# Optimization experiments

Hardware: AMD Instinct MI355X
Metric: run time of the kernel (lower is better)

## Reference

```python
import jax, jax.numpy as jnp
import numpy as np

N, E, F_IN, D, L = 100000, 1600000, 32, 128, 5
B, V, T, EMB = 3000, 64, 128, 64
H = L * D  # 640 LSTM hidden
BN_EPS = 1e-5


def setup_inputs():
    key = jax.random.key(0)
    ks = jax.random.split(key, 20)
    rn = lambda k, s, sc=0.05: jax.random.normal(k, s, jnp.float32) * sc
    inp = {
        'x': jax.random.normal(ks[0], (N, F_IN), jnp.float32),
        'edge_index': jax.random.randint(ks[1], (2, E), 0, N, jnp.int32),
        'batch': jnp.sort(jax.random.randint(ks[2], (N,), 0, B, jnp.int32)),
        'smi': jax.random.randint(ks[3], (B, T), 0, V, jnp.int32),
        'gin0_w1': rn(ks[4], (F_IN, D)), 'gin0_b1': jnp.zeros((D,), jnp.float32),
        'gin0_w2': rn(ks[5], (D, D)),    'gin0_b2': jnp.zeros((D,), jnp.float32),
        'ginr_w1': rn(ks[6], (L - 1, D, D)), 'ginr_b1': jnp.zeros((L - 1, D), jnp.float32),
        'ginr_w2': rn(ks[7], (L - 1, D, D)), 'ginr_b2': jnp.zeros((L - 1, D), jnp.float32),
        'bn_gamma': jnp.ones((L, D), jnp.float32), 'bn_beta': jnp.zeros((L, D), jnp.float32),
        'emb': rn(ks[8], (V, EMB), 0.1).at[0].set(0.0),  # padding_idx=0
        'w_ih': rn(ks[9], (4 * H, EMB), 0.04), 'w_hh': rn(ks[10], (4 * H, H), 0.04),
        'b_ih': jnp.zeros((4 * H,), jnp.float32), 'b_hh': jnp.zeros((4 * H,), jnp.float32),
        'g_w1': rn(ks[11], (L * D, 4 * D)), 'g_b1': jnp.zeros((4 * D,), jnp.float32),
        'g_bn_gamma': jnp.ones((4 * D,), jnp.float32), 'g_bn_beta': jnp.zeros((4 * D,), jnp.float32),
        'g_w2': rn(ks[12], (4 * D, 6 * D)),
    }
    return inp


def _bn(h, gamma, beta):
    # BatchNorm1d in training mode: biased batch statistics
    mu = h.mean(0)
    var = h.var(0)
    return (h - mu) * jax.lax.rsqrt(var + BN_EPS) * gamma + beta


def _gin_layer(h, src, dst, w1, b1, w2, b2, gamma, beta):
    # GINConv (eps=0): MLP(x + sum_{j->i} x_j), then ReLU, then BN
    agg = jax.ops.segment_sum(h[src], dst, num_segments=N)  # [N, d]
    z = h + agg
    z = jnp.maximum(z @ w1 + b1, 0.0) @ w2 + b2
    z = jnp.maximum(z, 0.0)
    return _bn(z, gamma, beta)


def _lstm_last(e, w_ih, w_hh, b_ih, b_hh):
    # e: [B, T, EMB] -> last hidden state [B, H]
    def step(carry, xt):
        h, c = carry
        gates = xt @ w_ih.T + b_ih + h @ w_hh.T + b_hh  # [B, 4H]
        i, f, g, o = jnp.split(gates, 4, axis=1)  # torch gate order i,f,g,o
        c = jax.nn.sigmoid(f) * c + jax.nn.sigmoid(i) * jnp.tanh(g)
        h = jax.nn.sigmoid(o) * jnp.tanh(c)
        return (h, c), None
    h0 = jnp.zeros((e.shape[0], H), e.dtype)
    (h, _), _ = jax.lax.scan(step, (h0, h0), e.transpose(1, 0, 2))
    return h


def reference(x, edge_index, batch, smi, gin0_w1, gin0_b1, gin0_w2, gin0_b2,
              ginr_w1, ginr_b1, ginr_w2, ginr_b2, bn_gamma, bn_beta, emb,
              w_ih, w_hh, b_ih, b_hh, g_w1, g_b1, g_bn_gamma, g_bn_beta, g_w2):
    src, dst = edge_index[0], edge_index[1]
    # --- GIN encoder with layer-wise global_add_pool ---
    h = _gin_layer(x, src, dst, gin0_w1, gin0_b1, gin0_w2, gin0_b2, bn_gamma[0], bn_beta[0])
    pools = [jax.ops.segment_sum(h, batch, num_segments=B)]
    for i in range(L - 1):
        h = _gin_layer(h, src, dst, ginr_w1[i], ginr_b1[i], ginr_w2[i], ginr_b2[i],
                       bn_gamma[i + 1], bn_beta[i + 1])
        pools.append(jax.ops.segment_sum(h, batch, num_segments=B))
    enc1 = jnp.concatenate(pools, axis=1)  # [B, L*D]
    # --- SMILES encoder: Embedding + LSTM, take output at last timestep ---
    enc2 = _lstm_last(emb[smi], w_ih, w_hh, b_ih, b_hh)  # [B, H] == [B, L*D]
    # --- shared projection head g, L2-normalized (F.normalize, eps=1e-12) ---
    def g_head(z):
        z1 = jnp.maximum(_bn(z @ g_w1 + g_b1, g_bn_gamma, g_bn_beta), 0.0)
        out = z1 @ g_w2
        nrm = jnp.maximum(jnp.linalg.norm(out, axis=1, keepdims=True), 1e-12)
        return out / nrm
    return (g_head(enc1), g_head(enc2))
```

## Files before the change

kernel.cpp:

```cpp
#include <hip/hip_runtime.h>

typedef __bf16 bf16x8 __attribute__((ext_vector_type(8)));
typedef float f32x4 __attribute__((ext_vector_type(4)));
typedef unsigned short ushort8 __attribute__((ext_vector_type(8)));

#define DEV static __device__ __forceinline__

DEV unsigned short f2bf(float f){
  unsigned int u = __builtin_bit_cast(unsigned int, f);
  u += 0x7fffu + ((u >> 16) & 1u);
  return (unsigned short)(u >> 16);
}
DEV float bf2f(unsigned short u){
  return __builtin_bit_cast(float, ((unsigned int)u) << 16);
}
DEV float sigf(float x){ return 1.0f/(1.0f + __expf(-x)); }
DEV float tanhf_fast(float x){
  float ax = fabsf(x);
  float e = __expf(2.0f*ax);
  float r = 1.0f - 2.0f/(e + 1.0f);
  return copysignf(r, x);
}

static constexpr int NN   = 100000;
static constexpr int NPAD = 100096;
static constexpr int NE   = 1600000;
static constexpr int NB   = 3000;
static constexpr int BPAD = 3072;
static constexpr int TT   = 128;
static constexpr int HID  = 640;
static constexpr int SCAN_B = 1024;
static constexpr int NBLK = (NN + SCAN_B - 1)/SCAN_B;

__global__ void cvt_k(const float* __restrict__ s, unsigned short* __restrict__ d, int n){
  int i = blockIdx.x*256 + threadIdx.x; if (i < n) d[i] = f2bf(s[i]);
}
__global__ void transpose_cvt_split_k(const float* __restrict__ s, unsigned short* __restrict__ dh,
                                      unsigned short* __restrict__ dl, int R, int C){
  int i = blockIdx.x*256 + threadIdx.x; if (i >= R*C) return;
  int r = i / C, c = i - r*C;
  float v = s[i];
  unsigned short hi = f2bf(v);
  dh[c*R + r] = hi;
  dl[c*R + r] = f2bf(v - bf2f(hi));
}
__global__ void wc2_build_k(const float* __restrict__ whh, const float* __restrict__ wih,
                            unsigned short* __restrict__ wc2){
  int i = blockIdx.x*256 + threadIdx.x; if (i >= 2560*704) return;
  int n2 = i / 704, k = i - n2*704;
  int jt = n2 >> 7, rem = n2 & 127;
  int hc = rem >> 6, gate = (rem >> 4) & 3, j15 = rem & 15;
  int n = gate*640 + jt*32 + hc*16 + j15;
  float v = (k < 640) ? whh[n*640 + k] : wih[n*64 + (k - 640)];
  wc2[i] = f2bf(v);
}
__global__ void add_k(const float* __restrict__ a, const float* __restrict__ b, float* __restrict__ o, int n){
  int i = blockIdx.x*256 + threadIdx.x; if (i < n) o[i] = a[i] + b[i];
}

__global__ __launch_bounds__(256) void deg_hist_k(const int* __restrict__ dsts, int* __restrict__ deg){
  int e = blockIdx.x*256 + threadIdx.x; if (e < NE) atomicAdd(&deg[dsts[e]], 1);
}
__global__ __launch_bounds__(256) void scan_bsum_k(const int* __restrict__ deg, int* __restrict__ bsum){
  __shared__ int red[4];
  int b = blockIdx.x, tid = threadIdx.x;
  int base = b*SCAN_B + tid*4;
  int s = 0;
  #pragma unroll
  for (int q = 0; q < 4; ++q){ int idx = base + q; s += (idx < NN) ? deg[idx] : 0; }
  #pragma unroll
  for (int m = 1; m < 64; m <<= 1) s += __shfl_xor(s, m);
  if ((tid & 63) == 0) red[tid >> 6] = s;
  __syncthreads();
  if (tid == 0) bsum[b] = red[0] + red[1] + red[2] + red[3];
}
__global__ void scan_off_k(int* __restrict__ bsum){
  if (threadIdx.x == 0){
    int run = 0;
    for (int i = 0; i < NBLK; ++i){ int t = bsum[i]; bsum[i] = run; run += t; }
  }
}
__global__ __launch_bounds__(256) void scan_write_k(const int* __restrict__ deg, const int* __restrict__ bsum,
                                                    int* __restrict__ rowptr, int* __restrict__ cursor){
  __shared__ int tsum[256];
  int b = blockIdx.x, tid = threadIdx.x;
  int base = b*SCAN_B + tid*4;
  int v[4]; int s = 0;
  #pragma unroll
  for (int q = 0; q < 4; ++q){ int idx = base + q; v[q] = (idx < NN) ? deg[idx] : 0; s += v[q]; }
  tsum[tid] = s;
  __syncthreads();
  for (int offt = 1; offt < 256; offt <<= 1){
    int y = (tid >= offt) ? tsum[tid - offt] : 0;
    __syncthreads();
    tsum[tid] += y;
    __syncthreads();
  }
  int run = bsum[b] + tsum[tid] - s;
  #pragma unroll
  for (int q = 0; q < 4; ++q){
    int idx = base + q;
    if (idx < NN){ rowptr[idx] = run; cursor[idx] = run; }
    run += v[q];
  }
  if (b == 0 && tid == 0) rowptr[NN] = NE;
}
__global__ __launch_bounds__(256) void csr_fill_k(const int* __restrict__ srcs, const int* __restrict__ dsts,
                                                  int* __restrict__ cursor, int* __restrict__ eidx){
  int e = blockIdx.x*256 + threadIdx.x; if (e >= NE) return;
  int d = dsts[e];
  int pos = atomicAdd(&cursor[d], 1);
  eidx[pos] = srcs[e];
}

__global__ __launch_bounds__(256) void gbound_k(const int* __restrict__ batch, int* __restrict__ gstart){
  int i = blockIdx.x*256 + threadIdx.x;
  if (i >= NN) return;
  int bi = batch[i];
  int bp = (i == 0) ? -1 : batch[i-1];
  for (int g = bp + 1; g <= bi; ++g) gstart[g] = i;
  if (i == NN-1){
    for (int g = bi + 1; g <= NB; ++g) gstart[g] = NN;
  }
}

__global__ __launch_bounds__(256) void agg128_k(const int* __restrict__ rowptr, const int* __restrict__ eidx,
    const float* __restrict__ H, float* __restrict__ Z){
  int wid = (blockIdx.x*256 + threadIdx.x) >> 6;
  if (wid >= NN) return;
  int lane = threadIdx.x & 63;
  const float2* Hp = (const float2*)H;
  int n0 = rowptr[wid], n1 = rowptr[wid+1];
  float2 acc = Hp[(size_t)wid*64 + lane];
  int i = n0;
  for (; i + 1 < n1; i += 2){
    int s0 = eidx[i], s1 = eidx[i+1];
    float2 v0 = Hp[(size_t)s0*64 + lane];
    float2 v1 = Hp[(size_t)s1*64 + lane];
    acc.x += v0.x + v1.x; acc.y += v0.y + v1.y;
  }
  if (i < n1){
    float2 v = Hp[(size_t)eidx[i]*64 + lane];
    acc.x += v.x; acc.y += v.y;
  }
  ((float2*)Z)[(size_t)wid*64 + lane] = acc;
}
__global__ __launch_bounds__(256) void agg32_k(const int* __restrict__ rowptr, const int* __restrict__ eidx,
    const float* __restrict__ X, float* __restrict__ Z){
  int r = (blockIdx.x*256 + threadIdx.x) >> 5;
  if (r >= NN) return;
  int l = threadIdx.x & 31;
  int n0 = rowptr[r], n1 = rowptr[r+1];
  float acc = X[(size_t)r*32 + l];
  int i = n0;
  for (; i + 1 < n1; i += 2){
    int s0 = eidx[i], s1 = eidx[i+1];
    acc += X[(size_t)s0*32 + l] + X[(size_t)s1*32 + l];
  }
  if (i < n1) acc += X[(size_t)eidx[i]*32 + l];
  Z[(size_t)r*32 + l] = acc;
}

template<int KIN>
__global__ __launch_bounds__(256) void gin_mlp_k(const float* __restrict__ Z,
    const unsigned short* __restrict__ W1h, const unsigned short* __restrict__ W1l,
    const unsigned short* __restrict__ W2h, const unsigned short* __restrict__ W2l,
    const float* __restrict__ b1, const float* __restrict__ b2,
    float* __restrict__ Y, float* __restrict__ stats)
{
  constexpr int SA = KIN + 8;
  __shared__ __align__(16) unsigned short Ah[128*136];
  __shared__ __align__(16) unsigned short Al[128*136];
  const int tid = threadIdx.x, lane = tid & 63, w = tid >> 6;
  const int row0 = blockIdx.x * 128;
  const int wr = (w >> 1)*64, wc0 = (w & 1)*64;
  const int l15 = lane & 15, lg = lane >> 4;

  constexpr int CH = KIN/8;
  #pragma unroll
  for (int i = 0; i < (128*CH)/256; ++i){
    int chunk = tid + 256*i;
    int row = chunk / CH, kc = (chunk - row*CH)*8;
    const float* sp = Z + (size_t)(row0 + row)*KIN + kc;
    float4 a0 = *(const float4*)sp;
    float4 a1 = *(const float4*)(sp + 4);
    float vv[8] = {a0.x,a0.y,a0.z,a0.w,a1.x,a1.y,a1.z,a1.w};
    ushort8 vh, vl;
    #pragma unroll
    for (int q=0;q<8;++q){ unsigned short h = f2bf(vv[q]); vh[q]=h; vl[q]=f2bf(vv[q]-bf2f(h)); }
    *(ushort8*)&Ah[row*SA + kc] = vh;
    *(ushort8*)&Al[row*SA + kc] = vl;
  }
  __syncthreads();

  f32x4 acc[4][4];
  #pragma unroll
  for (int i=0;i<4;++i)
    #pragma unroll
    for (int j=0;j<4;++j) acc[i][j] = (f32x4)(0.0f);

  #pragma unroll
  for (int k0 = 0; k0 < KIN; k0 += 32){
    bf16x8 ah[4], al[4], bh[4], bl[4];
    #pragma unroll
    for (int fa=0; fa<4; ++fa){
      ah[fa] = *(const bf16x8*)&Ah[(wr + fa*16 + l15)*SA + k0 + 8*lg];
      al[fa] = *(const bf16x8*)&Al[(wr + fa*16 + l15)*SA + k0 + 8*lg];
    }
    #pragma unroll
    for (int fb=0; fb<4; ++fb){
      bh[fb] = *(const bf16x8*)&W1h[(wc0 + fb*16 + l15)*KIN + k0 + 8*lg];
      bl[fb] = *(const bf16x8*)&W1l[(wc0 + fb*16 + l15)*KIN + k0 + 8*lg];
    }
    #pragma unroll
    for (int fa=0; fa<4; ++fa)
      #pragma unroll
      for (int fb=0; fb<4; ++fb){
        acc[fa][fb] = __builtin_amdgcn_mfma_f32_16x16x32_bf16(ah[fa], bh[fb], acc[fa][fb], 0, 0, 0);
        acc[fa][fb] = __builtin_amdgcn_mfma_f32_16x16x32_bf16(al[fa], bh[fb], acc[fa][fb], 0, 0, 0);
        acc[fa][fb] = __builtin_amdgcn_mfma_f32_16x16x32_bf16(ah[fa], bl[fb], acc[fa][fb], 0, 0, 0);
      }
  }
  __syncthreads();

  {
    float b1v[4];
    #pragma unroll
    for (int fb=0; fb<4; ++fb) b1v[fb] = b1[wc0 + fb*16 + l15];
    #pragma unroll
    for (int fa=0; fa<4; ++fa)
      #pragma unroll
      for (int fb=0; fb<4; ++fb)
        #pragma unroll
        for (int r=0; r<4; ++r){
          float v = fmaxf(acc[fa][fb][r] + b1v[fb], 0.0f);
          unsigned short h = f2bf(v);
          int idx = (wr + fa*16 + lg*4 + r)*136 + (wc0 + fb*16 + l15);
          Ah[idx] = h;
          Al[idx] = f2bf(v - bf2f(h));
        }
  }
  __syncthreads();

  f32x4 acc2[4][4];
  #pragma unroll
  for (int i=0;i<4;++i)
    #pragma unroll
    for (int j=0;j<4;++j) acc2[i][j] = (f32x4)(0.0f);

  #pragma unroll
  for (int k0 = 0; k0 < 128; k0 += 32){
    bf16x8 ah[4], al[4], bh[4], bl[4];
    #pragma unroll
    for (int fa=0; fa<4; ++fa){
      ah[fa] = *(const bf16x8*)&Ah[(wr + fa*16 + l15)*136 + k0 + 8*lg];
      al[fa] = *(const bf16x8*)&Al[(wr + fa*16 + l15)*136 + k0 + 8*lg];
    }
    #pragma unroll
    for (int fb=0; fb<4; ++fb){
      bh[fb] = *(const bf16x8*)&W2h[(wc0 + fb*16 + l15)*128 + k0 + 8*lg];
      bl[fb] = *(const bf16x8*)&W2l[(wc0 + fb*16 + l15)*128 + k0 + 8*lg];
    }
    #pragma unroll
    for (int fa=0; fa<4; ++fa)
      #pragma unroll
      for (int fb=0; fb<4; ++fb){
        acc2[fa][fb] = __builtin_amdgcn_mfma_f32_16x16x32_bf16(ah[fa], bh[fb], acc2[fa][fb], 0, 0, 0);
        acc2[fa][fb] = __builtin_amdgcn_mfma_f32_16x16x32_bf16(al[fa], bh[fb], acc2[fa][fb], 0, 0, 0);
        acc2[fa][fb] = __builtin_amdgcn_mfma_f32_16x16x32_bf16(ah[fa], bl[fb], acc2[fa][fb], 0, 0, 0);
      }
  }

  float b2v[4]; int cc[4];
  #pragma unroll
  for (int fb=0; fb<4; ++fb){ cc[fb] = wc0 + fb*16 + l15; b2v[fb] = b2[cc[fb]]; }
  float ps[4] = {0,0,0,0}, pq[4] = {0,0,0,0};
  #pragma unroll
  for (int fa=0; fa<4; ++fa)
    #pragma unroll
    for (int fb=0; fb<4; ++fb)
      #pragma unroll
      for (int r=0; r<4; ++r){
        int row = row0 + wr + fa*16 + lg*4 + r;
        float v = fmaxf(acc2[fa][fb][r] + b2v[fb], 0.0f);
        if (row < NN){
          Y[(size_t)row*128 + cc[fb]] = v;
          ps[fb] += v; pq[fb] += v*v;
        }
      }
  #pragma unroll
  for (int fb=0; fb<4; ++fb){
    float s = ps[fb]; s += __shfl_xor(s, 16); s += __shfl_xor(s, 32);
    float q = pq[fb]; q += __shfl_xor(q, 16); q += __shfl_xor(q, 32);
    if (lane < 16){ atomicAdd(&stats[cc[fb]], s); atomicAdd(&stats[128 + cc[fb]], q); }
  }
}

__global__ void bn_finalize_k(const float* __restrict__ stats, const float* __restrict__ gamma,
                              const float* __restrict__ beta, float* __restrict__ sshift, int C, float invN){
  int c = blockIdx.x*blockDim.x + threadIdx.x; if (c >= C) return;
  float mean = stats[c]*invN;
  float var  = fmaxf(stats[C+c]*invN - mean*mean, 0.0f);
  float inv  = rsqrtf(var + 1e-5f);
  float sc   = gamma[c]*inv;
  sshift[c] = sc; sshift[C+c] = beta[c] - mean*sc;
}

__global__ __launch_bounds__(256) void bn_apply_k(const float* __restrict__ Y,
    const float* __restrict__ sshift, float* __restrict__ Hb)
{
  int gid = blockIdx.x*256 + threadIdx.x;
  int r = gid >> 5;
  if (r >= NN) return;
  int c0 = (gid & 31) << 2;
  float4 y = *(const float4*)&Y[(size_t)r*128 + c0];
  float4 h;
  h.x = y.x*sshift[c0+0] + sshift[128+c0+0];
  h.y = y.y*sshift[c0+1] + sshift[128+c0+1];
  h.z = y.z*sshift[c0+2] + sshift[128+c0+2];
  h.w = y.w*sshift[c0+3] + sshift[128+c0+3];
  *(float4*)&Hb[(size_t)r*128 + c0] = h;
}

__global__ __launch_bounds__(256) void pool_seg_k(const float* __restrict__ Hb,
    const int* __restrict__ gstart, float* __restrict__ pool, int layer)
{
  int g = blockIdx.x*4 + (threadIdx.x >> 6);
  if (g >= NB) return;
  int lane = threadIdx.x & 63;
  int n0 = gstart[g], n1 = gstart[g+1];
  const float2* Hp = (const float2*)Hb;
  float2 acc = make_float2(0.f, 0.f);
  for (int r = n0; r < n1; ++r){
    float2 v = Hp[(size_t)r*64 + lane];
    acc.x += v.x; acc.y += v.y;
  }
  ((float2*)pool)[(size_t)g*320 + layer*64 + lane] = acc;
}

__global__ __launch_bounds__(256) void embed_k(const int* __restrict__ smi,
    const unsigned short* __restrict__ emb_bf, unsigned short* __restrict__ e2){
  int gid = blockIdx.x*256 + threadIdx.x;
  int tb = gid >> 4;
  if (tb >= TT*BPAD) return;
  int t = tb / BPAD, b = tb - t*BPAD;
  int k4 = (gid & 15) << 2;
  uint2 v = make_uint2(0u, 0u);
  if (b < NB){
    int tok = smi[b*TT + t];
    v = *(const uint2*)&emb_bf[tok*64 + k4];
  }
  *(uint2*)&e2[(size_t)tb*64 + k4] = v;
}

__global__ __launch_bounds__(512) void lstm_step_k(const unsigned short* __restrict__ hprev,
    unsigned short* __restrict__ hnext, float* __restrict__ cbuf,
    const unsigned short* __restrict__ e2, const unsigned short* __restrict__ Wc2,
    const float* __restrict__ biasc, int t, float* __restrict__ hfin)
{
  __shared__ __align__(16) unsigned short As[2][256*40];
  __shared__ __align__(16) unsigned short Bs[2][128*40];
  const int tid = threadIdx.x, lane = tid & 63, w = tid >> 6;
  const int row0 = blockIdx.x * 256;
  const int jt = blockIdx.y;
  const int l15 = lane & 15, lg = lane >> 4;
  const int wr = (w >> 1)*64, wc0 = (w & 1)*64;

  const int srow = tid >> 2, skc = (tid & 3) << 3;
  const unsigned short* A0 = hprev + (size_t)(row0 + srow)*HID;
  const unsigned short* A1 = hprev + (size_t)(row0 + srow + 128)*HID;
  const unsigned short* E0 = e2 + ((size_t)t*BPAD + row0 + srow)*64;
  const unsigned short* E1 = e2 + ((size_t)t*BPAD + row0 + srow + 128)*64;
  const unsigned short* B0 = Wc2 + (size_t)(jt*128 + srow)*704;

  *(ushort8*)&As[0][srow*40 + skc]       = *(const ushort8*)&A0[skc];
  *(ushort8*)&As[0][(srow+128)*40 + skc] = *(const ushort8*)&A1[skc];
  *(ushort8*)&Bs[0][srow*40 + skc]       = *(const ushort8*)&B0[skc];
  __syncthreads();

  f32x4 acc[4][4];
  #pragma unroll
  for (int i=0;i<4;++i)
    #pragma unroll
    for (int j=0;j<4;++j) acc[i][j] = (f32x4)(0.0f);

  int p = 0;
  for (int kk = 0; kk < 22; ++kk){
    ushort8 va0, va1, vb0;
    const int k1 = (kk+1)*32;
    if (kk < 21){
      if (k1 < 640){
        va0 = *(const ushort8*)&A0[k1 + skc];
        va1 = *(const ushort8*)&A1[k1 + skc];
      } else {
        va0 = *(const ushort8*)&E0[k1 - 640 + skc];
        va1 = *(const ushort8*)&E1[k1 - 640 + skc];
      }
      vb0 = *(const ushort8*)&B0[k1 + skc];
    }
    bf16x8 a[4], b[4];
    #pragma unroll
    for (int fa=0; fa<4; ++fa) a[fa] = *(const bf16x8*)&As[p][(wr + fa*16 + l15)*40 + 8*lg];
    #pragma unroll
    for (int fb=0; fb<4; ++fb) b[fb] = *(const bf16x8*)&Bs[p][(wc0 + fb*16 + l15)*40 + 8*lg];
    #pragma unroll
    for (int fa=0; fa<4; ++fa)
      #pragma unroll
      for (int fb=0; fb<4; ++fb)
        acc[fa][fb] = __builtin_amdgcn_mfma_f32_16x16x32_bf16(a[fa], b[fb], acc[fa][fb], 0, 0, 0);
    if (kk < 21){
      *(ushort8*)&As[p^1][srow*40 + skc]       = va0;
      *(ushort8*)&As[p^1][(srow+128)*40 + skc] = va1;
      *(ushort8*)&Bs[p^1][srow*40 + skc]       = vb0;
    }
    __syncthreads();
    p ^= 1;
  }

  const int j = jt*32 + (w & 1)*16 + l15;
  float bi = biasc[j], bf_ = biasc[640+j], bg = biasc[1280+j], bo = biasc[1920+j];
  #pragma unroll
  for (int fa=0; fa<4; ++fa){
    #pragma unroll
    for (int r=0; r<4; ++r){
      int br = row0 + wr + fa*16 + lg*4 + r;
      float iv = acc[fa][0][r] + bi;
      float fv = acc[fa][1][r] + bf_;
      float gv = acc[fa][2][r] + bg;
      float ov = acc[fa][3][r] + bo;
      size_t idx = (size_t)br*HID + j;
      float co = cbuf[idx];
      float cn = sigf(fv)*co + sigf(iv)*tanhf_fast(gv);
      cbuf[idx] = cn;
      float hv = sigf(ov)*tanhf_fast(cn);
      hnext[idx] = f2bf(hv);
      if (hfin) hfin[idx] = hv;
    }
  }
}

template<int DO_STATS>
__global__ __launch_bounds__(256) void gemm_split_k(const float* __restrict__ A,
    const unsigned short* __restrict__ Bh, const unsigned short* __restrict__ Bl,
    const float* __restrict__ bias, float* __restrict__ outp, float* __restrict__ stats,
    int Mvalid, int Nc, int K)
{
  __shared__ __align__(16) unsigned short Ah[128*40];
  __shared__ __align__(16) unsigned short Al[128*40];
  const int tid = threadIdx.x, lane = tid & 63, w = tid >> 6;
  const int row0 = blockIdx.x * 128, col0 = blockIdx.y * 128;
  const int wr = (w >> 1)*64, wc0 = (w & 1)*64;
  const int l15 = lane & 15, lg = lane >> 4;

  f32x4 acc[4][4];
  #pragma unroll
  for (int i=0;i<4;++i)
    #pragma unroll
    for (int j=0;j<4;++j) acc[i][j] = (f32x4)(0.0f);

  for (int k0 = 0; k0 < K; k0 += 32){
    #pragma unroll
    for (int i=0;i<2;++i){
      int chunk = tid + 256*i;
      int row = chunk >> 2, kc = (chunk & 3) << 3;
      const float* sp = A + (size_t)(row0+row)*K + k0 + kc;
      float4 a0 = *(const float4*)sp;
      float4 a1 = *(const float4*)(sp + 4);
      float vv[8] = {a0.x,a0.y,a0.z,a0.w,a1.x,a1.y,a1.z,a1.w};
      ushort8 vh, vl;
      #pragma unroll
      for (int q=0;q<8;++q){ unsigned short h = f2bf(vv[q]); vh[q]=h; vl[q]=f2bf(vv[q]-bf2f(h)); }
      *(ushort8*)&Ah[row*40 + kc] = vh;
      *(ushort8*)&Al[row*40 + kc] = vl;
    }
    __syncthreads();
    bf16x8 ah[4], al[4], bh[4], bl[4];
    #pragma unroll
    for (int fa=0; fa<4; ++fa){
      ah[fa] = *(const bf16x8*)&Ah[(wr + fa*16 + l15)*40 + 8*lg];
      al[fa] = *(const bf16x8*)&Al[(wr + fa*16 + l15)*40 + 8*lg];
    }
    #pragma unroll
    for (int fb=0; fb<4; ++fb){
      bh[fb] = *(const bf16x8*)&Bh[(size_t)(col0 + wc0 + fb*16 + l15)*K + k0 + 8*lg];
      bl[fb] = *(const bf16x8*)&Bl[(size_t)(col0 + wc0 + fb*16 + l15)*K + k0 + 8*lg];
    }
    #pragma unroll
    for (int fa=0; fa<4; ++fa)
      #pragma unroll
      for (int fb=0; fb<4; ++fb){
        acc[fa][fb] = __builtin_amdgcn_mfma_f32_16x16x32_bf16(ah[fa], bh[fb], acc[fa][fb], 0, 0, 0);
        acc[fa][fb] = __builtin_amdgcn_mfma_f32_16x16x32_bf16(al[fa], bh[fb], acc[fa][fb], 0, 0, 0);
        acc[fa][fb] = __builtin_amdgcn_mfma_f32_16x16x32_bf16(ah[fa], bl[fb], acc[fa][fb], 0, 0, 0);
      }
    __syncthreads();
  }

  float bv[4]; int cc[4];
  #pragma unroll
  for (int fb=0; fb<4; ++fb){ cc[fb] = col0 + wc0 + fb*16 + l15; bv[fb] = bias ? bias[cc[fb]] : 0.0f; }
  float ps[4] = {0,0,0,0}, pq[4] = {0,0,0,0};
  #pragma unroll
  for (int fa=0; fa<4; ++fa)
    #pragma unroll
    for (int fb=0; fb<4; ++fb)
      #pragma unroll
      for (int r=0; r<4; ++r){
        int row = row0 + wr + fa*16 + lg*4 + r;
        float v = acc[fa][fb][r] + bv[fb];
        if (row < Mvalid){
          outp[(size_t)row*Nc + cc[fb]] = v;
          if (DO_STATS){ ps[fb] += v; pq[fb] += v*v; }
        }
      }
  if (DO_STATS){
    #pragma unroll
    for (int fb=0; fb<4; ++fb){
      float s = ps[fb]; s += __shfl_xor(s, 16); s += __shfl_xor(s, 32);
      float q = pq[fb]; q += __shfl_xor(q, 16); q += __shfl_xor(q, 32);
      if (lane < 16){ atomicAdd(&stats[cc[fb]], s); atomicAdd(&stats[Nc + cc[fb]], q); }
    }
  }
}

__global__ __launch_bounds__(256) void bn_apply_head_k(const float* __restrict__ Zpre,
    const float* __restrict__ sshift, float* __restrict__ z1f){
  int gid = blockIdx.x*256 + threadIdx.x;
  int r = gid >> 7;
  if (r >= BPAD) return;
  int c0 = (gid & 127) << 2;
  float4 o = make_float4(0.f,0.f,0.f,0.f);
  if (r < NB){
    float4 v = *(const float4*)&Zpre[(size_t)r*512 + c0];
    o.x = fmaxf(v.x*sshift[c0+0] + sshift[512+c0+0], 0.0f);
    o.y = fmaxf(v.y*sshift[c0+1] + sshift[512+c0+1], 0.0f);
    o.z = fmaxf(v.z*sshift[c0+2] + sshift[512+c0+2], 0.0f);
    o.w = fmaxf(v.w*sshift[c0+3] + sshift[512+c0+3], 0.0f);
  }
  *(float4*)&z1f[(size_t)r*512 + c0] = o;
}

__global__ __launch_bounds__(256) void rownorm_k(const float* __restrict__ in, float* __restrict__ outp){
  int r = blockIdx.x;
  const float* p = in + (size_t)r*768;
  float ss = 0.0f;
  #pragma unroll
  for (int i = 0; i < 3; ++i){ float v = p[threadIdx.x + 256*i]; ss += v*v; }
  #pragma unroll
  for (int m = 1; m < 64; m <<= 1) ss += __shfl_xor(ss, m);
  __shared__ float red[4];
  if ((threadIdx.x & 63) == 0) red[threadIdx.x >> 6] = ss;
  __syncthreads();
  float tot = red[0] + red[1] + red[2] + red[3];
  float inv = 1.0f / fmaxf(sqrtf(tot), 1e-12f);
  float* q = outp + (size_t)r*768;
  #pragma unroll
  for (int i = 0; i < 3; ++i) q[threadIdx.x + 256*i] = p[threadIdx.x + 256*i]*inv;
}

static inline int cdiv(long a, long b){ return (int)((a + b - 1)/b); }

extern "C" void kernel_launch(void* const* d_in, const int* in_sizes, int n_in,
                              void* d_out, int out_size, void* d_ws, size_t ws_size,
                              hipStream_t stream)
{
  const float* x        = (const float*)d_in[0];
  const int*   edges    = (const int*)d_in[1];
  const int*   batch    = (const int*)d_in[2];
  const int*   smi      = (const int*)d_in[3];
  const float* gin0_w1  = (const float*)d_in[4];
  const float* gin0_b1  = (const float*)d_in[5];
  const float* gin0_w2  = (const float*)d_in[6];
  const float* gin0_b2  = (const float*)d_in[7];
  const float* ginr_w1  = (const float*)d_in[8];
  const float* ginr_b1  = (const float*)d_in[9];
  const float* ginr_w2  = (const float*)d_in[10];
  const float* ginr_b2  = (const float*)d_in[11];
  const float* bn_gamma = (const float*)d_in[12];
  const float* bn_beta  = (const float*)d_in[13];
  const float* emb      = (const float*)d_in[14];
  const float* w_ih     = (const float*)d_in[15];
  const float* w_hh     = (const float*)d_in[16];
  const float* b_ih     = (const float*)d_in[17];
  const float* b_hh     = (const float*)d_in[18];
  const float* g_w1     = (const float*)d_in[19];
  const float* g_b1     = (const float*)d_in[20];
  const float* g_bng    = (const float*)d_in[21];
  const float* g_bnb    = (const float*)d_in[22];
  const float* g_w2     = (const float*)d_in[23];
  float* outp = (float*)d_out;
  const int* srcs = edges;
  const int* dsts = edges + NE;

  char* base = (char*)d_ws;
  size_t off = 0;
  auto carve = [&](size_t bytes)->char*{ char* p = base + off; off += (bytes + 255) & ~(size_t)255; return p; };
  float* z_gin = (float*)carve((size_t)NPAD*128*4);
  float* y_gin = (float*)carve((size_t)NPAD*128*4);
  float* h_gin = (float*)carve((size_t)NPAD*128*4);
  float* pool  = (float*)carve((size_t)BPAD*HID*4);
  unsigned short* Wc2    = (unsigned short*)carve((size_t)2560*704*2);
  float*          biasc  = (float*)carve(2560*4);
  unsigned short* emb_bf = (unsigned short*)carve(4096*2);
  unsigned short* w1t0h  = (unsigned short*)carve(128*32*2);
  unsigned short* w1t0l  = (unsigned short*)carve(128*32*2);
  unsigned short* w2t0h  = (unsigned short*)carve(128*128*2);
  unsigned short* w2t0l  = (unsigned short*)carve(128*128*2);
  unsigned short* w1trh  = (unsigned short*)carve(4*16384*2);
  unsigned short* w1trl  = (unsigned short*)carve(4*16384*2);
  unsigned short* w2trh  = (unsigned short*)carve(4*16384*2);
  unsigned short* w2trl  = (unsigned short*)carve(4*16384*2);
  unsigned short* gw1th  = (unsigned short*)carve(512*640*2);
  unsigned short* gw1tl  = (unsigned short*)carve(512*640*2);
  unsigned short* gw2th  = (unsigned short*)carve(768*512*2);
  unsigned short* gw2tl  = (unsigned short*)carve(768*512*2);
  float* stats  = (float*)carve(1024*4);
  float* sshift = (float*)carve(1024*4);
  int* deg    = (int*)carve((size_t)NN*4);
  int* cursor = (int*)carve((size_t)NN*4);
  int* rowptr = (int*)carve((size_t)(NN+1)*4);
  int* bsum   = (int*)carve(512);
  int* eidx   = (int*)carve((size_t)NE*4);
  int* gstart = (int*)carve((size_t)(NB+1)*4);

  unsigned short* e2     = (unsigned short*)y_gin;
  unsigned short* h_a    = (unsigned short*)h_gin;
  unsigned short* h_b    = h_a + (size_t)BPAD*HID;
  float*          c_buf  = (float*)(h_b + (size_t)BPAD*HID);
  float*          hfin   = c_buf + (size_t)BPAD*HID;
  float*          z1pre  = (float*)z_gin;
  float*          z1f    = z1pre + (size_t)BPAD*512;
  float*          outtmp = z1f + (size_t)BPAD*512;

  wc2_build_k<<<cdiv((long)2560*704,256),256,0,stream>>>(w_hh, w_ih, Wc2);
  add_k<<<cdiv(2560,256),256,0,stream>>>(b_ih, b_hh, biasc, 2560);
  cvt_k<<<cdiv(4096,256),256,0,stream>>>(emb, emb_bf, 4096);
  transpose_cvt_split_k<<<cdiv(32*128,256),256,0,stream>>>(gin0_w1, w1t0h, w1t0l, 32, 128);
  transpose_cvt_split_k<<<cdiv(16384,256),256,0,stream>>>(gin0_w2, w2t0h, w2t0l, 128, 128);
  for (int i = 0; i < 4; ++i){
    transpose_cvt_split_k<<<cdiv(16384,256),256,0,stream>>>(ginr_w1 + (size_t)i*16384, w1trh + (size_t)i*16384, w1trl + (size_t)i*16384, 128, 128);
    transpose_cvt_split_k<<<cdiv(16384,256),256,0,stream>>>(ginr_w2 + (size_t)i*16384, w2trh + (size_t)i*16384, w2trl + (size_t)i*16384, 128, 128);
  }
  transpose_cvt_split_k<<<cdiv(640*512,256),256,0,stream>>>(g_w1, gw1th, gw1tl, 640, 512);
  transpose_cvt_split_k<<<cdiv(512*768,256),256,0,stream>>>(g_w2, gw2th, gw2tl, 512, 768);

  hipMemsetAsync(deg, 0, (size_t)NN*4, stream);
  deg_hist_k<<<cdiv(NE,256),256,0,stream>>>(dsts, deg);
  scan_bsum_k<<<NBLK,256,0,stream>>>(deg, bsum);
  scan_off_k<<<1,64,0,stream>>>(bsum);
  scan_write_k<<<NBLK,256,0,stream>>>(deg, bsum, rowptr, cursor);
  csr_fill_k<<<cdiv(NE,256),256,0,stream>>>(srcs, dsts, cursor, eidx);
  gbound_k<<<cdiv(NN,256),256,0,stream>>>(batch, gstart);

  for (int l = 0; l < 5; ++l){
    hipMemsetAsync(stats, 0, 1024*4, stream);
    if (l == 0)
      agg32_k<<<cdiv((long)NN*32,256),256,0,stream>>>(rowptr, eidx, x, z_gin);
    else
      agg128_k<<<cdiv((long)NN*64,256),256,0,stream>>>(rowptr, eidx, h_gin, z_gin);
    if (l == 0)
      gin_mlp_k<32><<<NPAD/128,256,0,stream>>>(z_gin, w1t0h, w1t0l, w2t0h, w2t0l, gin0_b1, gin0_b2, y_gin, stats);
    else
      gin_mlp_k<128><<<NPAD/128,256,0,stream>>>(z_gin, w1trh + (size_t)(l-1)*16384, w1trl + (size_t)(l-1)*16384,
                                                w2trh + (size_t)(l-1)*16384, w2trl + (size_t)(l-1)*16384,
                                                ginr_b1 + (l-1)*128, ginr_b2 + (l-1)*128, y_gin, stats);
    bn_finalize_k<<<1,128,0,stream>>>(stats, bn_gamma + l*128, bn_beta + l*128, sshift, 128, 1.0f/NN);
    bn_apply_k<<<cdiv((long)NN*32,256),256,0,stream>>>(y_gin, sshift, h_gin);
    pool_seg_k<<<cdiv(NB,4),256,0,stream>>>(h_gin, gstart, pool, l);
  }

  embed_k<<<cdiv((long)TT*BPAD*16,256),256,0,stream>>>(smi, emb_bf, e2);
  hipMemsetAsync(h_a, 0, (size_t)BPAD*HID*2, stream);
  hipMemsetAsync(c_buf, 0, (size_t)BPAD*HID*4, stream);
  for (int t = 0; t < TT; ++t){
    const unsigned short* hin = (t & 1) ? h_b : h_a;
    unsigned short* hout      = (t & 1) ? h_a : h_b;
    lstm_step_k<<<dim3(BPAD/256, 20),512,0,stream>>>(hin, hout, c_buf, e2, Wc2, biasc, t,
                                                     (t == TT-1) ? hfin : nullptr);
  }

  const float* headAf[2] = { pool, hfin };
  for (int hd = 0; hd < 2; ++hd){
    hipMemsetAsync(stats, 0, 1024*4, stream);
    gemm_split_k<1><<<dim3(BPAD/128, 4),256,0,stream>>>(headAf[hd], gw1th, gw1tl, g_b1, z1pre, stats, NB, 512, 640);
    bn_finalize_k<<<2,256,0,stream>>>(stats, g_bng, g_bnb, sshift, 512, 1.0f/NB);
    bn_apply_head_k<<<cdiv((long)BPAD*128,256),256,0,stream>>>(z1pre, sshift, z1f);
    gemm_split_k<0><<<dim3(BPAD/128, 6),256,0,stream>>>(z1f, gw2th, gw2tl, nullptr, outtmp, nullptr, NB, 768, 512);
    rownorm_k<<<NB,256,0,stream>>>(outtmp, outp + (size_t)hd*NB*768);
  }
}
```

Baseline: 4.914 ms.

## Replace per-timestep LSTM launches with a persistent cooperative kernel using grid sync

The 128 per-timestep LSTM kernel launches become a single cooperative persistent kernel of 240 blocks that loops over time and calls grid.sync between steps. The cell state now lives in registers instead of a global buffer, which removes its global reads and writes and the memset. The tile shape changes to 128 rows by 256 gate columns, with the weight layout reordered to match. The costs are a grid-wide barrier per step, the requirement that all 240 blocks are co-resident (two 512-thread blocks per CU), and each block re-streaming its weight slice from cache at every step.

```diff
diff --git a/kernel.cpp b/kernel.cpp
--- a/kernel.cpp
+++ b/kernel.cpp
@@ -1,4 +1,6 @@
 #include <hip/hip_runtime.h>
+#include <hip/hip_cooperative_groups.h>
+namespace cg = cooperative_groups;
 
 typedef __bf16 bf16x8 __attribute__((ext_vector_type(8)));
 typedef float f32x4 __attribute__((ext_vector_type(4)));
@@ -44,15 +46,15 @@
   dh[c*R + r] = hi;
   dl[c*R + r] = f2bf(v - bf2f(hi));
 }
-__global__ void wc2_build_k(const float* __restrict__ whh, const float* __restrict__ wih,
-                            unsigned short* __restrict__ wc2){
+__global__ void wc3_build_k(const float* __restrict__ whh, const float* __restrict__ wih,
+                            unsigned short* __restrict__ wc3){
   int i = blockIdx.x*256 + threadIdx.x; if (i >= 2560*704) return;
   int n2 = i / 704, k = i - n2*704;
-  int jt = n2 >> 7, rem = n2 & 127;
+  int jt = n2 >> 8, rem = n2 & 255;
   int hc = rem >> 6, gate = (rem >> 4) & 3, j15 = rem & 15;
-  int n = gate*640 + jt*32 + hc*16 + j15;
+  int n = gate*640 + jt*64 + hc*16 + j15;
   float v = (k < 640) ? whh[n*640 + k] : wih[n*64 + (k - 640)];
-  wc2[i] = f2bf(v);
+  wc3[i] = f2bf(v);
 }
 __global__ void add_k(const float* __restrict__ a, const float* __restrict__ b, float* __restrict__ o, int n){
   int i = blockIdx.x*256 + threadIdx.x; if (i < n) o[i] = a[i] + b[i];
@@ -353,89 +355,102 @@
   *(uint2*)&e2[(size_t)tb*64 + k4] = v;
 }
 
-__global__ __launch_bounds__(512) void lstm_step_k(const unsigned short* __restrict__ hprev,
-    unsigned short* __restrict__ hnext, float* __restrict__ cbuf,
-    const unsigned short* __restrict__ e2, const unsigned short* __restrict__ Wc2,
-    const float* __restrict__ biasc, int t, float* __restrict__ hfin)
+__global__ __launch_bounds__(512,2) void lstm_persist_k(
+    unsigned short* __restrict__ ha, unsigned short* __restrict__ hb,
+    const unsigned short* __restrict__ e2, const unsigned short* __restrict__ Wc3,
+    const float* __restrict__ biasc, float* __restrict__ hfin)
 {
-  __shared__ __align__(16) unsigned short As[2][256*40];
-  __shared__ __align__(16) unsigned short Bs[2][128*40];
+  cg::grid_group grid = cg::this_grid();
+  __shared__ __align__(16) unsigned short As[2][128*40];
+  __shared__ __align__(16) unsigned short Bs[2][256*40];
   const int tid = threadIdx.x, lane = tid & 63, w = tid >> 6;
-  const int row0 = blockIdx.x * 256;
-  const int jt = blockIdx.y;
+  const int bid = blockIdx.x;
+  const int rt = bid % 24, jt = bid / 24;
+  const int row0 = rt*128;
   const int l15 = lane & 15, lg = lane >> 4;
-  const int wr = (w >> 1)*64, wc0 = (w & 1)*64;
+  const int wr = (w >> 2)*64, wc0 = (w & 3)*64;
 
   const int srow = tid >> 2, skc = (tid & 3) << 3;
-  const unsigned short* A0 = hprev + (size_t)(row0 + srow)*HID;
-  const unsigned short* A1 = hprev + (size_t)(row0 + srow + 128)*HID;
-  const unsigned short* E0 = e2 + ((size_t)t*BPAD + row0 + srow)*64;
-  const unsigned short* E1 = e2 + ((size_t)t*BPAD + row0 + srow + 128)*64;
-  const unsigned short* B0 = Wc2 + (size_t)(jt*128 + srow)*704;
-
-  *(ushort8*)&As[0][srow*40 + skc]       = *(const ushort8*)&A0[skc];
-  *(ushort8*)&As[0][(srow+128)*40 + skc] = *(const ushort8*)&A1[skc];
-  *(ushort8*)&Bs[0][srow*40 + skc]       = *(const ushort8*)&B0[skc];
-  __syncthreads();
-
-  f32x4 acc[4][4];
+  const int brow = tid >> 1, bkc = (tid & 1) << 4;
+  const unsigned short* Bp = Wc3 + (size_t)(jt*256 + brow)*704;
+
+  const int j = jt*64 + (w & 3)*16 + l15;
+  const float bi  = biasc[j];
+  const float bff = biasc[640 + j];
+  const float bg  = biasc[1280 + j];
+  const float bo  = biasc[1920 + j];
+
+  float creg[4][4];
   #pragma unroll
   for (int i=0;i<4;++i)
     #pragma unroll
-    for (int j=0;j<4;++j) acc[i][j] = (f32x4)(0.0f);
-
-  int p = 0;
-  for (int kk = 0; kk < 22; ++kk){
-    ushort8 va0, va1, vb0;
-    const int k1 = (kk+1)*32;
-    if (kk < 21){
-      if (k1 < 640){
-        va0 = *(const ushort8*)&A0[k1 + skc];
-        va1 = *(const ushort8*)&A1[k1 + skc];
-      } else {
-        va0 = *(const ushort8*)&E0[k1 - 640 + skc];
-        va1 = *(const ushort8*)&E1[k1 - 640 + skc];
+    for (int r=0;r<4;++r) creg[i][r] = 0.0f;
+
+  unsigned short* hbuf[2] = { ha, hb };
+
+  for (int t = 0; t < TT; ++t){
+    const unsigned short* hcur = hbuf[t & 1];
+    unsigned short* hnxt = hbuf[(t & 1) ^ 1];
+    const unsigned short* Arow = hcur + (size_t)(row0 + srow)*HID;
+    const unsigned short* Erow = e2 + ((size_t)t*BPAD + row0 + srow)*64;
+
+    *(ushort8*)&As[0][srow*40 + skc] = *(const ushort8*)&Arow[skc];
+    *(ushort8*)&Bs[0][brow*40 + bkc]     = *(const ushort8*)&Bp[bkc];
+    *(ushort8*)&Bs[0][brow*40 + bkc + 8] = *(const ushort8*)&Bp[bkc + 8];
+    __syncthreads();
+
+    f32x4 acc[4][4];
+    #pragma unroll
+    for (int i=0;i<4;++i)
+      #pragma unroll
+      for (int q=0;q<4;++q) acc[i][q] = (f32x4)(0.0f);
+
+    int p = 0;
+    for (int kk = 0; kk < 22; ++kk){
+      ushort8 va, vb0, vb1;
+      const int k1 = (kk+1)*32;
+      if (kk < 21){
+        va  = (k1 < 640) ? *(const ushort8*)&Arow[k1 + skc]
+                         : *(const ushort8*)&Erow[k1 - 640 + skc];
+        vb0 = *(const ushort8*)&Bp[k1 + bkc];
+        vb1 = *(const ushort8*)&Bp[k1 + bkc + 8];
       }
-      vb0 = *(const ushort8*)&B0[k1 + skc];
-    }
-    bf16x8 a[4], b[4];
-    #pragma unroll
-    for (int fa=0; fa<4; ++fa) a[fa] = *(const bf16x8*)&As[p][(wr + fa*16 + l15)*40 + 8*lg];
-    #pragma unroll
-    for (int fb=0; fb<4; ++fb) b[fb] = *(const bf16x8*)&Bs[p][(wc0 + fb*16 + l15)*40 + 8*lg];
-    #pragma unroll
-    for (int fa=0; fa<4; ++fa)
-      #pragma unroll
-      for (int fb=0; fb<4; ++fb)
-        acc[fa][fb] = __builtin_amdgcn_mfma_f32_16x16x32_bf16(a[fa], b[fb], acc[fa][fb], 0, 0, 0);
-    if (kk < 21){
-      *(ushort8*)&As[p^1][srow*40 + skc]       = va0;
-      *(ushort8*)&As[p^1][(srow+128)*40 + skc] = va1;
-      *(ushort8*)&Bs[p^1][srow*40 + skc]       = vb0;
-    }
-    __syncthreads();
-    p ^= 1;
-  }
-
-  const int j = jt*32 + (w & 1)*16 + l15;
-  float bi = biasc[j], bf_ = biasc[640+j], bg = biasc[1280+j], bo = biasc[1920+j];
-  #pragma unroll
-  for (int fa=0; fa<4; ++fa){
-    #pragma unroll
-    for (int r=0; r<4; ++r){
-      int br = row0 + wr + fa*16 + lg*4 + r;
-      float iv = acc[fa][0][r] + bi;
-      float fv = acc[fa][1][r] + bf_;
-      float gv = acc[fa][2][r] + bg;
-      float ov = acc[fa][3][r] + bo;
-      size_t idx = (size_t)br*HID + j;
-      float co = cbuf[idx];
-      float cn = sigf(fv)*co + sigf(iv)*tanhf_fast(gv);
-      cbuf[idx] = cn;
-      float hv = sigf(ov)*tanhf_fast(cn);
-      hnext[idx] = f2bf(hv);
-      if (hfin) hfin[idx] = hv;
-    }
+      bf16x8 a[4], b[4];
+      #pragma unroll
+      for (int fa=0; fa<4; ++fa) a[fa] = *(const bf16x8*)&As[p][(wr + fa*16 + l15)*40 + 8*lg];
+      #pragma unroll
+      for (int fb=0; fb<4; ++fb) b[fb] = *(const bf16x8*)&Bs[p][(wc0 + fb*16 + l15)*40 + 8*lg];
+      #pragma unroll
+      for (int fa=0; fa<4; ++fa)
+        #pragma unroll
+        for (int fb=0; fb<4; ++fb)
+          acc[fa][fb] = __builtin_amdgcn_mfma_f32_16x16x32_bf16(a[fa], b[fb], acc[fa][fb], 0, 0, 0);
+      if (kk < 21){
+        *(ushort8*)&As[p^1][srow*40 + skc] = va;
+        *(ushort8*)&Bs[p^1][brow*40 + bkc]     = vb0;
+        *(ushort8*)&Bs[p^1][brow*40 + bkc + 8] = vb1;
+      }
+      __syncthreads();
+      p ^= 1;
+    }
+
+    #pragma unroll
+    for (int fa=0; fa<4; ++fa){
+      #pragma unroll
+      for (int r=0; r<4; ++r){
+        int br = row0 + wr + fa*16 + lg*4 + r;
+        float iv = acc[fa][0][r] + bi;
+        float fv = acc[fa][1][r] + bff;
+        float gv = acc[fa][2][r] + bg;
+        float ov = acc[fa][3][r] + bo;
+        float cn = sigf(fv)*creg[fa][r] + sigf(iv)*tanhf_fast(gv);
+        creg[fa][r] = cn;
+        float hv = sigf(ov)*tanhf_fast(cn);
+        if (t == TT-1) hfin[(size_t)br*HID + j] = hv;
+        else           hnxt[(size_t)br*HID + j] = f2bf(hv);
+      }
+    }
+    if (t < TT-1) grid.sync();
   }
 }
 
@@ -599,7 +614,7 @@
   float* y_gin = (float*)carve((size_t)NPAD*128*4);
   float* h_gin = (float*)carve((size_t)NPAD*128*4);
   float* pool  = (float*)carve((size_t)BPAD*HID*4);
-  unsigned short* Wc2    = (unsigned short*)carve((size_t)2560*704*2);
+  unsigned short* Wc3    = (unsigned short*)carve((size_t)2560*704*2);
   float*          biasc  = (float*)carve(2560*4);
   unsigned short* emb_bf = (unsigned short*)carve(4096*2);
   unsigned short* w1t0h  = (unsigned short*)carve(128*32*2);
@@ -626,13 +641,13 @@
   unsigned short* e2     = (unsigned short*)y_gin;
   unsigned short* h_a    = (unsigned short*)h_gin;
   unsigned short* h_b    = h_a + (size_t)BPAD*HID;
-  float*          c_buf  = (float*)(h_b + (size_t)BPAD*HID);
-  float*          hfin   = c_buf + (size_t)BPAD*HID;
+  float*          c_spare= (float*)(h_b + (size_t)BPAD*HID);
+  float*          hfin   = c_spare + (size_t)BPAD*HID;
   float*          z1pre  = (float*)z_gin;
   float*          z1f    = z1pre + (size_t)BPAD*512;
   float*          outtmp = z1f + (size_t)BPAD*512;
 
-  wc2_build_k<<<cdiv((long)2560*704,256),256,0,stream>>>(w_hh, w_ih, Wc2);
+  wc3_build_k<<<cdiv((long)2560*704,256),256,0,stream>>>(w_hh, w_ih, Wc3);
   add_k<<<cdiv(2560,256),256,0,stream>>>(b_ih, b_hh, biasc, 2560);
   cvt_k<<<cdiv(4096,256),256,0,stream>>>(emb, emb_bf, 4096);
   transpose_cvt_split_k<<<cdiv(32*128,256),256,0,stream>>>(gin0_w1, w1t0h, w1t0l, 32, 128);
@@ -671,12 +686,9 @@
 
   embed_k<<<cdiv((long)TT*BPAD*16,256),256,0,stream>>>(smi, emb_bf, e2);
   hipMemsetAsync(h_a, 0, (size_t)BPAD*HID*2, stream);
-  hipMemsetAsync(c_buf, 0, (size_t)BPAD*HID*4, stream);
-  for (int t = 0; t < TT; ++t){
-    const unsigned short* hin = (t & 1) ? h_b : h_a;
-    unsigned short* hout      = (t & 1) ? h_a : h_b;
-    lstm_step_k<<<dim3(BPAD/256, 20),512,0,stream>>>(hin, hout, c_buf, e2, Wc2, biasc, t,
-                                                     (t == TT-1) ? hfin : nullptr);
+  {
+    void* kargs[] = { (void*)&h_a, (void*)&h_b, (void*)&e2, (void*)&Wc3, (void*)&biasc, (void*)&hfin };
+    hipLaunchCooperativeKernel((const void*)lstm_persist_k, dim3(240), dim3(512), kargs, 0, stream);
   }
 
   const float* headAf[2] = { pool, hfin };
```

Result: slower. 8.017 ms (+63.2%).
